# Performance work log

Hardware: AMD Instinct MI355X
Metric: run time of the kernel (lower is better)

The kernel has to match this reference:

```python
import jax, jax.numpy as jnp
import numpy as np

# Per-field categorical vocab sizes (order matches torch ModuleDict insertion order)
VOCABS = np.array([100000, 800, 200, 5000, 60, 30000, 10, 8, 50, 2000, 20, 16], dtype=np.int64)
OFFSETS = np.concatenate([[0], np.cumsum(VOCABS)[:-1]]).astype(np.int64)  # start row of each field
V_TOTAL = int(VOCABS.sum())
PADDING_IDX = 0
B, L, C, F, D = 64, 512, len(VOCABS), 4, 128


def setup_inputs() -> dict:
    key = jax.random.key(0)
    k_cat, k_cont, k_tab, k_w, k_b = jax.random.split(key, 5)
    # indices per field in [0, vocab_f)
    cat = jax.random.randint(k_cat, (B, L, C), 0, jnp.asarray(VOCABS))
    cont = jax.random.normal(k_cont, (B, L, F), dtype=jnp.float32)
    # all C embedding tables concatenated row-wise into one fused table [V_total, D]
    table = jax.random.normal(k_tab, (V_TOTAL, D), dtype=jnp.float32)
    # nn.Linear(1, D): weight [D,1] -> store as [F, D]; bias [F, D]
    bound = 1.0  # 1/sqrt(in_features=1)
    w_cont = jax.random.uniform(k_w, (F, D), dtype=jnp.float32, minval=-bound, maxval=bound)
    b_cont = jax.random.uniform(k_b, (F, D), dtype=jnp.float32, minval=-bound, maxval=bound)
    return {"cat": cat, "cont": cont, "table": table, "w_cont": w_cont, "b_cont": b_cont}


def reference(cat, cont, table, w_cont, b_cont):
    # zero the padding row of every field's sub-table (torch padding_idx semantics)
    pad_rows = jnp.asarray(OFFSETS) + PADDING_IDX
    table_eff = table.at[pad_rows].set(0.0)
    # fused multi-table gather: shift each field's indices into the concatenated table
    idx = cat + jnp.asarray(OFFSETS)[None, None, :]          # [B, L, C]
    cat_emb = table_eff[idx]                                  # [B, L, C, D]
    # per-field Linear(1, D): x * w_f + b_f, batched over all F fields
    cont_emb = cont[..., None] * w_cont[None, None] + b_cont[None, None]  # [B, L, F, D]
    tokens = jnp.concatenate([cat_emb, cont_emb], axis=2)     # [B, L, C+F, D]
    Bq, Lq = cat.shape[0], cat.shape[1]
    return tokens.reshape(Bq * Lq, C + F, D)
```

## Files before the change

kernel.cpp:

```cpp
#include <hip/hip_runtime.h>

#define C_FIELDS 12
#define F_FIELDS 4
#define SLOTS    16
#define D_DIM    128

using f32x4 = __attribute__((ext_vector_type(4))) float;

__global__ __launch_bounds__(256) void emb_fused_kernel(
    const int*   __restrict__ cat,
    const float* __restrict__ cont,
    const float* __restrict__ table,
    const float* __restrict__ wc,
    const float* __restrict__ bc,
    float*       __restrict__ out,
    int n_tok)
{
    const int gtid  = blockIdx.x * blockDim.x + threadIdx.x;
    int token = gtid >> 6;
    if (token >= n_tok) return;
    token = __builtin_amdgcn_readfirstlane(token);

    const int lane = threadIdx.x & 63;
    const int hi   = lane >> 5;
    const int seg  = lane & 31;
    const int d0   = seg << 2;

    constexpr int OFFS[C_FIELDS] = {
        0, 100000, 100800, 101000, 106000, 106060,
        136060, 136070, 136078, 136128, 138128, 138148
    };

    const int*   catrow  = cat  + token * C_FIELDS;
    const float* controw = cont + token * F_FIELDS;
    int sidx[C_FIELDS];
#pragma unroll
    for (int c = 0; c < C_FIELDS; ++c) sidx[c] = catrow[c];
    float sx[F_FIELDS];
#pragma unroll
    for (int f = 0; f < F_FIELDS; ++f) sx[f] = controw[f];

    int idxs[6];
    const float* ptrs[6];
#pragma unroll
    for (int k = 0; k < 6; ++k) {
        const int idx = hi ? sidx[2 * k + 1] : sidx[2 * k];
        const int off = hi ? OFFS[2 * k + 1] : OFFS[2 * k];
        idxs[k] = idx;
        ptrs[k] = table + (size_t)(off + idx) * D_DIM + d0;
    }

    f32x4 v[6];
#pragma unroll
    for (int k = 0; k < 6; ++k) {
        v[k] = *reinterpret_cast<const f32x4*>(ptrs[k]);
    }

    f32x4 rc[2];
#pragma unroll
    for (int k = 0; k < 2; ++k) {
        const int   f = 2 * k + hi;
        const float x = hi ? sx[2 * k + 1] : sx[2 * k];
        const f32x4 wv = *reinterpret_cast<const f32x4*>(wc + f * D_DIM + d0);
        const f32x4 bv = *reinterpret_cast<const f32x4*>(bc + f * D_DIM + d0);
        rc[k].x = fmaf(x, wv.x, bv.x);
        rc[k].y = fmaf(x, wv.y, bv.y);
        rc[k].z = fmaf(x, wv.z, bv.z);
        rc[k].w = fmaf(x, wv.w, bv.w);
    }

#pragma unroll
    for (int k = 0; k < 6; ++k) {
        const f32x4 z = {0.f, 0.f, 0.f, 0.f};
        v[k] = (idxs[k] == 0) ? z : v[k];
    }

    float* out_tok = out + (size_t)token * (SLOTS * D_DIM);
#pragma unroll
    for (int k = 0; k < 6; ++k) {
        __builtin_nontemporal_store(
            v[k], reinterpret_cast<f32x4*>(out_tok + (2 * k + hi) * D_DIM + d0));
    }
#pragma unroll
    for (int k = 0; k < 2; ++k) {
        __builtin_nontemporal_store(
            rc[k], reinterpret_cast<f32x4*>(out_tok + (12 + 2 * k + hi) * D_DIM + d0));
    }
}

extern "C" void kernel_launch(void* const* d_in, const int* in_sizes, int n_in,
                              void* d_out, int out_size, void* d_ws, size_t ws_size,
                              hipStream_t stream) {
    const int*   cat   = (const int*)d_in[0];
    const float* cont  = (const float*)d_in[1];
    const float* table = (const float*)d_in[2];
    const float* wc    = (const float*)d_in[3];
    const float* bc    = (const float*)d_in[4];
    float*       out   = (float*)d_out;

    const int n_tok = in_sizes[0] / C_FIELDS;
    const long long total_threads = (long long)n_tok * 64;
    const int block = 256;
    const int grid  = (int)((total_threads + block - 1) / block);

    emb_fused_kernel<<<grid, block, 0, stream>>>(cat, cont, table, wc, bc, out, n_tok);
}
```

Before: 354.6 us.

## Convert embedding gather to persistent grid-stride waves with prefetched indices

Launches a capped grid of 2048 blocks. Each wave loops over tokens with a grid stride, loading the Linear weights and biases once per wave. While the current token's rows are still being stored, the next token's categorical indices and continuous values are prefetched. Padding rows are masked with a float multiply instead of a select, and row offsets use 32-bit arithmetic. The loop should overlap scalar-load latency and amortise setup, but fewer waves in flight may reduce memory-level parallelism for a bandwidth-bound gather.

```diff
diff --git a/kernel.cpp b/kernel.cpp
--- a/kernel.cpp
+++ b/kernel.cpp
@@ -16,75 +16,90 @@
     float*       __restrict__ out,
     int n_tok)
 {
-    const int gtid  = blockIdx.x * blockDim.x + threadIdx.x;
-    int token = gtid >> 6;
-    if (token >= n_tok) return;
-    token = __builtin_amdgcn_readfirstlane(token);
-
-    const int lane = threadIdx.x & 63;
-    const int hi   = lane >> 5;
-    const int seg  = lane & 31;
-    const int d0   = seg << 2;
-
     constexpr int OFFS[C_FIELDS] = {
         0, 100000, 100800, 101000, 106000, 106060,
         136060, 136070, 136078, 136128, 138128, 138148
     };
 
-    const int*   catrow  = cat  + token * C_FIELDS;
-    const float* controw = cont + token * F_FIELDS;
-    int sidx[C_FIELDS];
+    const int lane = threadIdx.x & 63;
+    const int hi   = lane >> 5;
+    const int d0   = (lane & 31) << 2;
+
+    const int wave0  = __builtin_amdgcn_readfirstlane(
+        (int)((blockIdx.x * blockDim.x + threadIdx.x) >> 6));
+    const int nwaves = (int)((gridDim.x * blockDim.x) >> 6);
+
+    f32x4 wv[2], bv[2];
 #pragma unroll
-    for (int c = 0; c < C_FIELDS; ++c) sidx[c] = catrow[c];
-    float sx[F_FIELDS];
-#pragma unroll
-    for (int f = 0; f < F_FIELDS; ++f) sx[f] = controw[f];
-
-    int idxs[6];
-    const float* ptrs[6];
-#pragma unroll
-    for (int k = 0; k < 6; ++k) {
-        const int idx = hi ? sidx[2 * k + 1] : sidx[2 * k];
-        const int off = hi ? OFFS[2 * k + 1] : OFFS[2 * k];
-        idxs[k] = idx;
-        ptrs[k] = table + (size_t)(off + idx) * D_DIM + d0;
+    for (int k = 0; k < 2; ++k) {
+        const int f = 2 * k + hi;
+        wv[k] = *reinterpret_cast<const f32x4*>(wc + f * D_DIM + d0);
+        bv[k] = *reinterpret_cast<const f32x4*>(bc + f * D_DIM + d0);
     }
 
-    f32x4 v[6];
+    int   sidx[C_FIELDS];
+    float sx[F_FIELDS];
+    auto load_scalars = [&](int token) {
+        const int*   catrow  = cat  + token * C_FIELDS;
+        const float* controw = cont + token * F_FIELDS;
 #pragma unroll
-    for (int k = 0; k < 6; ++k) {
-        v[k] = *reinterpret_cast<const f32x4*>(ptrs[k]);
-    }
+        for (int c = 0; c < C_FIELDS; ++c) sidx[c] = catrow[c];
+#pragma unroll
+        for (int f = 0; f < F_FIELDS; ++f) sx[f] = controw[f];
+    };
 
-    f32x4 rc[2];
+    int token = wave0;
+    if (token >= n_tok) return;
+    load_scalars(token);
+
+    while (true) {
+        uint32_t voff[6];
+        float    fmask[6];
 #pragma unroll
-    for (int k = 0; k < 2; ++k) {
-        const int   f = 2 * k + hi;
-        const float x = hi ? sx[2 * k + 1] : sx[2 * k];
-        const f32x4 wv = *reinterpret_cast<const f32x4*>(wc + f * D_DIM + d0);
-        const f32x4 bv = *reinterpret_cast<const f32x4*>(bc + f * D_DIM + d0);
-        rc[k].x = fmaf(x, wv.x, bv.x);
-        rc[k].y = fmaf(x, wv.y, bv.y);
-        rc[k].z = fmaf(x, wv.z, bv.z);
-        rc[k].w = fmaf(x, wv.w, bv.w);
-    }
+        for (int k = 0; k < 6; ++k) {
+            const uint32_t re = (uint32_t)(OFFS[2*k]   + sidx[2*k])   * (uint32_t)D_DIM;
+            const uint32_t ro = (uint32_t)(OFFS[2*k+1] + sidx[2*k+1]) * (uint32_t)D_DIM;
+            voff[k] = (hi ? ro : re) + (uint32_t)d0;
+            const float fe = (sidx[2*k]   != 0) ? 1.f : 0.f;
+            const float fo = (sidx[2*k+1] != 0) ? 1.f : 0.f;
+            fmask[k] = hi ? fo : fe;
+        }
+
+        f32x4 v[6];
+#pragma unroll
+        for (int k = 0; k < 6; ++k)
+            v[k] = *reinterpret_cast<const f32x4*>(table + voff[k]);
+
+        f32x4 rc[2];
+#pragma unroll
+        for (int k = 0; k < 2; ++k) {
+            const float x = hi ? sx[2*k+1] : sx[2*k];
+            rc[k].x = fmaf(x, wv[k].x, bv[k].x);
+            rc[k].y = fmaf(x, wv[k].y, bv[k].y);
+            rc[k].z = fmaf(x, wv[k].z, bv[k].z);
+            rc[k].w = fmaf(x, wv[k].w, bv[k].w);
+        }
+
+        float* outp = out + (size_t)token * (SLOTS * D_DIM) + hi * D_DIM + d0;
+
+        const int  next = token + nwaves;
+        const bool more = next < n_tok;
+        if (more) load_scalars(next);
 
 #pragma unroll
-    for (int k = 0; k < 6; ++k) {
-        const f32x4 z = {0.f, 0.f, 0.f, 0.f};
-        v[k] = (idxs[k] == 0) ? z : v[k];
-    }
+        for (int k = 0; k < 6; ++k) {
+            f32x4 r = v[k];
+            r.x *= fmask[k]; r.y *= fmask[k]; r.z *= fmask[k]; r.w *= fmask[k];
+            __builtin_nontemporal_store(
+                r, reinterpret_cast<f32x4*>(outp + k * (2 * D_DIM)));
+        }
+#pragma unroll
+        for (int k = 0; k < 2; ++k)
+            __builtin_nontemporal_store(
+                rc[k], reinterpret_cast<f32x4*>(outp + (C_FIELDS + 2 * k) * D_DIM));
 
-    float* out_tok = out + (size_t)token * (SLOTS * D_DIM);
-#pragma unroll
-    for (int k = 0; k < 6; ++k) {
-        __builtin_nontemporal_store(
-            v[k], reinterpret_cast<f32x4*>(out_tok + (2 * k + hi) * D_DIM + d0));
-    }
-#pragma unroll
-    for (int k = 0; k < 2; ++k) {
-        __builtin_nontemporal_store(
-            rc[k], reinterpret_cast<f32x4*>(out_tok + (12 + 2 * k + hi) * D_DIM + d0));
+        if (!more) break;
+        token = next;
     }
 }
 
@@ -99,9 +114,11 @@
     float*       out   = (float*)d_out;
 
     const int n_tok = in_sizes[0] / C_FIELDS;
-    const long long total_threads = (long long)n_tok * 64;
+
     const int block = 256;
-    const int grid  = (int)((total_threads + block - 1) / block);
+    int grid = (n_tok + 3) / 4;
+    if (grid > 2048) grid = 2048;
+    if (grid < 1)    grid = 1;
 
     emb_fused_kernel<<<grid, block, 0, stream>>>(cat, cont, table, wc, bc, out, n_tok);
 }
```

After: 351.4 us. No clear change (-0.9%).
